# Kernel optimization log

Hardware: AMD Instinct MI355X
Metric: run time of the kernel (lower is better)

Reference implementation:

```python
import jax, jax.numpy as jnp
import numpy as np

EMBED_DIM = 2048
NUM_HEADS = 32
NUM_SEQS = 8
SEQ_LEN = 1024
TOTAL_TOKENS = NUM_SEQS * SEQ_LEN


def setup_inputs() -> dict:
    key = jax.random.key(0)
    ks = jax.random.split(key, 9)
    E = EMBED_DIM
    std = 0.02
    return {
        "hidden_states": jax.random.normal(ks[0], (TOTAL_TOKENS, E), dtype=jnp.float32),
        "Wq": jax.random.normal(ks[1], (E, E), dtype=jnp.float32) * std,
        "bq": jax.random.normal(ks[2], (E,), dtype=jnp.float32) * std,
        "Wk": jax.random.normal(ks[3], (E, E), dtype=jnp.float32) * std,
        "bk": jax.random.normal(ks[4], (E,), dtype=jnp.float32) * std,
        "Wv": jax.random.normal(ks[5], (E, E), dtype=jnp.float32) * std,
        "bv": jax.random.normal(ks[6], (E,), dtype=jnp.float32) * std,
        "Wo": jax.random.normal(ks[7], (E, E), dtype=jnp.float32) * std,
        "bo": jax.random.normal(ks[8], (E,), dtype=jnp.float32) * std,
        "seq_len": SEQ_LEN,
    }


def reference(hidden_states, Wq, bq, Wk, bk, Wv, bv, Wo, bo, seq_len):
    # OPTAttention (has_cache=False): block-diagonal causal attention over
    # packed ragged sequences; here all NUM_SEQS sequences have length seq_len,
    # so the block-diagonal mask is exactly per-sequence causal attention.
    T, E = hidden_states.shape
    H = NUM_HEADS
    D = E // H
    B = T // seq_len
    scaling = D ** -0.5

    # torch nn.Linear: y = x @ W.T + b
    q = hidden_states @ Wq.T + bq
    k = hidden_states @ Wk.T + bk
    v = hidden_states @ Wv.T + bv

    q = q.reshape(B, seq_len, H, D)
    k = k.reshape(B, seq_len, H, D)
    v = v.reshape(B, seq_len, H, D)

    # [B, H, S, S] attention scores (xformers applies scale to q@k.T)
    scores = jnp.einsum("bqhd,bkhd->bhqk", q, k) * scaling
    causal = jnp.tril(jnp.ones((seq_len, seq_len), dtype=bool))
    scores = jnp.where(causal[None, None, :, :], scores, jnp.finfo(scores.dtype).min)
    probs = jax.nn.softmax(scores, axis=-1)

    attn = jnp.einsum("bhqk,bkhd->bqhd", probs, v)  # [B, S, H, D]
    attn = attn.reshape(T, E)
    return attn @ Wo.T + bo
```

## Files before the change

### kernel.cpp

```cpp
#include <hip/hip_runtime.h>
#include <hip/hip_bf16.h>

typedef __bf16 bf16_t;
typedef __bf16 bf16x8 __attribute__((ext_vector_type(8)));
typedef __bf16 bf16x4 __attribute__((ext_vector_type(4)));
typedef float f32x4 __attribute__((ext_vector_type(4)));
typedef float f32x16 __attribute__((ext_vector_type(16)));
typedef unsigned short u16x8 __attribute__((ext_vector_type(8)));
typedef unsigned int u32x4 __attribute__((ext_vector_type(4)));

#define T_TOK 8192
#define E_DIM 2048
#define NHEAD 32
#define SEQLEN 1024
#define NSEQ 8
#define LDQ 6144

#if __has_builtin(__builtin_amdgcn_exp2f)
#define EXP2F(x) __builtin_amdgcn_exp2f(x)
#else
#define EXP2F(x) exp2f(x)
#endif

static __device__ inline unsigned cvtpk_bf16(float lo, float hi) {
    unsigned r;
    asm("v_cvt_pk_bf16_f32 %0, %1, %2" : "=v"(r) : "v"(lo), "v"(hi));
    return r;
}

static __device__ inline void plswap(unsigned &x, unsigned &y, bool lo_half) {
#if __has_builtin(__builtin_amdgcn_permlane32_swap)
    auto r = __builtin_amdgcn_permlane32_swap(x, y, false, false);
    x = r[0]; y = r[1];
#else
    unsigned xs = __shfl_xor(x, 32), ys = __shfl_xor(y, 32);
    unsigned nx = lo_half ? x : ys;
    unsigned ny = lo_half ? xs : y;
    x = nx; y = ny;
#endif
}

__global__ void cvt_all(const float* __restrict__ hid, const float* __restrict__ Wq,
                        const float* __restrict__ Wk, const float* __restrict__ Wv,
                        const float* __restrict__ Wo, bf16_t* __restrict__ hidB,
                        bf16_t* __restrict__ Wcat, bf16_t* __restrict__ WoB) {
    const int TE4 = (T_TOK * E_DIM) / 4;
    const int EE4 = (E_DIM * E_DIM) / 4;
    const float* src;
    bf16_t* dst;
    int n4, base, nb;
    const int bid = blockIdx.x;
    if (bid < 2048)      { src = hid; dst = hidB;              n4 = TE4; base = 0;    nb = 2048; }
    else if (bid < 2560) { src = Wq;  dst = Wcat;              n4 = EE4; base = 2048; nb = 512; }
    else if (bid < 3072) { src = Wk;  dst = Wcat + 4 * EE4;    n4 = EE4; base = 2560; nb = 512; }
    else if (bid < 3584) { src = Wv;  dst = Wcat + 8 * EE4;    n4 = EE4; base = 3072; nb = 512; }
    else                 { src = Wo;  dst = WoB;               n4 = EE4; base = 3584; nb = 512; }
    const int stride = nb * 256;
    for (int i = (bid - base) * 256 + threadIdx.x; i < n4; i += stride) {
        const float4 v = reinterpret_cast<const float4*>(src)[i];
        bf16x4 o;
        o[0] = (bf16_t)v.x; o[1] = (bf16_t)v.y; o[2] = (bf16_t)v.z; o[3] = (bf16_t)v.w;
        reinterpret_cast<bf16x4*>(dst)[i] = o;
    }
}

template<bool OUT_BF16>
__global__ __launch_bounds__(512, 2)
void gemm64(const bf16_t* __restrict__ A, const bf16_t* __restrict__ B,
            const float* __restrict__ b0, const float* __restrict__ b1,
            const float* __restrict__ b2, void* __restrict__ Cout,
            int M, int N, float qs, int qlim) {
    constexpr int K = 2048;
    constexpr int NK = K / 64;
    __shared__ alignas(16) unsigned char lds[131072];
    const int tid = threadIdx.x;
    const int wid = tid >> 6, l = tid & 63;
    const int cpx = gridDim.x >> 3;
    const int id = (blockIdx.x & 7) * cpx + (blockIdx.x >> 3);
    const int sb = id >> 5, si = id & 31;
    const int smw = (M >> 8) >> 3;
    const int bm = (sb % smw) * 8 + (si & 7);
    const int bn = (sb / smw) * 4 + (si >> 3);
    const int wrow = (wid >> 2) * 128, wcol = (wid & 3) * 64;
    const int lr = l & 15, lg = l >> 4;

    f32x4 acc[8][4] = {};

    const bf16_t* aBase = A + (size_t)(bm * 256) * K;
    const bf16_t* bBase = B + (size_t)(bn * 256) * K;

    const int srw = l >> 3;
    const int scb0 = (l & 7) * 16;
    auto stage = [&](int t, int buf) {
        unsigned char* base = lds + buf * 65536;
#pragma unroll
        for (int i = 0; i < 4; ++i) {
            const int chunk = wid * 4 + i;
            const int r = chunk * 8 + srw;
            const int cb = scb0 ^ ((r & 7) << 4);
            __builtin_amdgcn_global_load_lds(
                (const __attribute__((address_space(1))) void*)(aBase + (size_t)r * K + t * 64 + (cb >> 1)),
                (__attribute__((address_space(3))) void*)(base + chunk * 1024), 16, 0, 0);
        }
#pragma unroll
        for (int i = 0; i < 4; ++i) {
            const int chunk = wid * 4 + i;
            const int r = chunk * 8 + srw;
            const int cb = scb0 ^ ((r & 7) << 4);
            __builtin_amdgcn_global_load_lds(
                (const __attribute__((address_space(1))) void*)(bBase + (size_t)r * K + t * 64 + (cb >> 1)),
                (__attribute__((address_space(3))) void*)(base + 32768 + chunk * 1024), 16, 0, 0);
        }
    };

    stage(0, 0);
    asm volatile("s_waitcnt vmcnt(0)" ::: "memory");
    __builtin_amdgcn_s_barrier();

#pragma unroll 1
    for (int t = 0; t < NK; ++t) {
        if (t + 1 < NK) stage(t + 1, (t + 1) & 1);
        const unsigned char* Ab = lds + (t & 1) * 65536;
        const unsigned char* Bb = Ab + 32768;
        bf16x8 af[8][2], bfv[4][2];
#pragma unroll
        for (int n = 0; n < 4; ++n) {
            const int r = wcol + n * 16 + lr;
#pragma unroll
            for (int ks = 0; ks < 2; ++ks)
                bfv[n][ks] = *reinterpret_cast<const bf16x8*>(
                    Bb + r * 128 + (((unsigned)(ks * 64 + lg * 16)) ^ ((r & 7) << 4)));
        }
#pragma unroll
        for (int m = 0; m < 8; ++m) {
            const int r = wrow + m * 16 + lr;
#pragma unroll
            for (int ks = 0; ks < 2; ++ks)
                af[m][ks] = *reinterpret_cast<const bf16x8*>(
                    Ab + r * 128 + (((unsigned)(ks * 64 + lg * 16)) ^ ((r & 7) << 4)));
        }
        __builtin_amdgcn_s_setprio(1);
#pragma unroll
        for (int m = 0; m < 8; ++m)
#pragma unroll
            for (int n = 0; n < 4; ++n)
#pragma unroll
                for (int ks = 0; ks < 2; ++ks)
                    acc[m][n] = __builtin_amdgcn_mfma_f32_16x16x32_bf16(af[m][ks], bfv[n][ks], acc[m][n], 0, 0, 0);
        __builtin_amdgcn_s_setprio(0);
        if (t == NK - 1) break;
        asm volatile("s_waitcnt vmcnt(0)" ::: "memory");
        __builtin_amdgcn_s_barrier();
    }

    const int r0 = bm * 256 + wrow + lg * 4;
    const int c0 = bn * 256 + wcol + lr;
#pragma unroll
    for (int n = 0; n < 4; ++n) {
        const int cc = c0 + n * 16;
        const float bias = (cc < 2048) ? b0[cc] : (cc < 4096 ? b1[cc - 2048] : b2[cc - 4096]);
        const float sc2 = (cc < qlim) ? qs : 1.0f;
#pragma unroll
        for (int m = 0; m < 8; ++m)
#pragma unroll
            for (int j = 0; j < 4; ++j) {
                const int rr = r0 + m * 16 + j;
                const float v = (acc[m][n][j] + bias) * sc2;
                if (OUT_BF16) ((bf16_t*)Cout)[(size_t)rr * N + cc] = (bf16_t)v;
                else          ((float*)Cout)[(size_t)rr * N + cc] = v;
            }
    }
}

__global__ __launch_bounds__(512, 2)
void attn_fwd3(const bf16_t* __restrict__ QKV, bf16_t* __restrict__ Og) {
    const int orig = blockIdx.x;
    const int id = (orig & 7) * 64 + (orig >> 3);
    const int grp = id >> 1;
    const int pairIdx = id & 1;
    const int h = grp & 31;
    const int sq = grp >> 5;

    const int tid = threadIdx.x;
    const int w = tid >> 6;
    const int l = tid & 63;
    const int ll = l & 31;
    const int hi = l >> 5;
    const bool lo_half = (hi == 0);

    __shared__ alignas(16) unsigned char lds[65536];

    const bf16_t* Qg = QKV;
    const bf16_t* Kg = QKV + 2048;
    const bf16_t* Vg = QKV + 4096;
    const size_t kvbase = (size_t)(sq * SEQLEN) * LDQ + h * 64;

    bf16x8 vr0, vr1;
    const int vk0 = l * 2;
    const int vd0 = w * 8;

    auto stageK = [&](int kt, int buf) {
#pragma unroll
        for (int c = 0; c < 2; ++c) {
            const int o = (w * 2 + c) * 1024 + l * 16;
            const int r = o >> 7;
            const int swb = (o & 127) ^ ((r & 7) << 4);
            const bf16_t* src = Kg + kvbase + (size_t)(kt * 128 + r) * LDQ + (swb >> 1);
            __builtin_amdgcn_global_load_lds(
                (const __attribute__((address_space(1))) void*)src,
                (__attribute__((address_space(3))) void*)(lds + buf * 16384 + (w * 2 + c) * 1024),
                16, 0, 0);
        }
    };
    auto loadV = [&](int kt) {
        const bf16_t* vp = Vg + kvbase + (size_t)(kt * 128 + vk0) * LDQ + vd0;
        vr0 = *reinterpret_cast<const bf16x8*>(vp);
        vr1 = *reinterpret_cast<const bf16x8*>(vp + LDQ);
    };
    auto writeV = [&](int buf) {
        u16x8 s0 = __builtin_bit_cast(u16x8, vr0);
        u16x8 s1 = __builtin_bit_cast(u16x8, vr1);
        unsigned char* vb = lds + 32768 + buf * 16384;
#pragma unroll
        for (int e = 0; e < 8; ++e) {
            const int d = vd0 + e;
            unsigned off = (unsigned)(d * 256 + vk0 * 2);
            off ^= ((unsigned)((d ^ (d >> 4)) & 15)) << 4;
            *reinterpret_cast<unsigned*>(vb + off) = (unsigned)s0[e] | ((unsigned)s1[e] << 16);
        }
    };

    const unsigned ksw = (unsigned)((l & 7) << 4);
    const unsigned kbase = (unsigned)(ll * 128 + hi * 16);

#pragma unroll 1
    for (int seg = 0; seg < 2; ++seg) {
        const int qt = pairIdx ? (seg ? 2 : 1) : (seg ? 3 : 0);

        const int q_glob = qt * 256 + w * 32 + ll;
        const bf16_t* qp = Qg + (size_t)(sq * SEQLEN + q_glob) * LDQ + h * 64 + hi * 8;
        bf16x8 qf[4];
#pragma unroll
        for (int dc = 0; dc < 4; ++dc)
            qf[dc] = *reinterpret_cast<const bf16x8*>(qp + dc * 16);

        const int nkt = 2 * qt + 2;
        const int q_wave_max = qt * 256 + w * 32 + 31;

        f32x16 oac[2] = {};
        float mrun = -3.0e38f, lsum = 0.f;

        stageK(0, 0);
        loadV(0);
        writeV(0);
        __syncthreads();

        int cur = 0;
        for (int kt = 0; kt < nkt; ++kt) {
            const bool notlast = (kt + 1 < nkt);
            if (notlast) { stageK(kt + 1, cur ^ 1); loadV(kt + 1); }

            if (kt * 128 <= q_wave_max) {
                const unsigned char* Kcur = lds + cur * 16384;
                const unsigned char* Vcur = lds + 32768 + cur * 16384;

                f32x16 st[4];
#pragma unroll
                for (int kh = 0; kh < 4; ++kh) {
                    f32x16 acc = {};
#pragma unroll
                    for (int dc = 0; dc < 4; ++dc) {
                        const unsigned off = (kbase + (unsigned)(kh * 4096 + dc * 32)) ^ ksw;
                        const bf16x8 ka = *reinterpret_cast<const bf16x8*>(Kcur + off);
                        acc = __builtin_amdgcn_mfma_f32_32x32x16_bf16(ka, qf[dc], acc, 0, 0, 0);
                    }
                    st[kh] = acc;
                }

                if (kt >= 2 * qt) {
#pragma unroll
                    for (int kh = 0; kh < 4; ++kh)
#pragma unroll
                        for (int r = 0; r < 16; ++r) {
                            const int kg = kt * 128 + kh * 32 + (r & 3) + 8 * (r >> 2) + 4 * hi;
                            if (kg > q_glob) st[kh][r] = -3.0e38f;
                        }
                }

                float tm = -3.0e38f;
#pragma unroll
                for (int kh = 0; kh < 4; ++kh)
#pragma unroll
                    for (int r = 0; r < 16; ++r) tm = fmaxf(tm, st[kh][r]);
                tm = fmaxf(tm, __shfl_xor(tm, 32));

                if (!__all(tm <= mrun + 8.0f)) {
                    const float mnew = fmaxf(mrun, tm);
                    const float rsc = EXP2F(mrun - mnew);
                    mrun = mnew;
                    lsum *= rsc;
#pragma unroll
                    for (int dh = 0; dh < 2; ++dh)
#pragma unroll
                        for (int r = 0; r < 16; ++r) oac[dh][r] *= rsc;
                }

                float ps = 0.f;
#pragma unroll
                for (int kh = 0; kh < 4; ++kh)
#pragma unroll
                    for (int r = 0; r < 16; ++r) {
                        const float p = EXP2F(st[kh][r] - mrun);
                        st[kh][r] = p;
                        ps += p;
                    }
                ps += __shfl_xor(ps, 32);
                lsum += ps;

                bf16x8 pf[8];
#pragma unroll
                for (int kh = 0; kh < 4; ++kh)
#pragma unroll
                    for (int hc = 0; hc < 2; ++hc) {
                        const int b0i = hc * 8;
                        unsigned a  = cvtpk_bf16(st[kh][b0i + 0], st[kh][b0i + 1]);
                        unsigned b  = cvtpk_bf16(st[kh][b0i + 4], st[kh][b0i + 5]);
                        unsigned a2 = cvtpk_bf16(st[kh][b0i + 2], st[kh][b0i + 3]);
                        unsigned b2 = cvtpk_bf16(st[kh][b0i + 6], st[kh][b0i + 7]);
                        plswap(a, b, lo_half);
                        plswap(a2, b2, lo_half);
                        u32x4 words = { a, a2, b, b2 };
                        pf[kh * 2 + hc] = __builtin_bit_cast(bf16x8, words);
                    }

#pragma unroll
                for (int dh = 0; dh < 2; ++dh) {
                    const int d = dh * 32 + ll;
                    const unsigned vsw = ((unsigned)((d ^ (d >> 4)) & 15)) << 4;
                    const unsigned vbb = (unsigned)(d * 256 + hi * 16);
#pragma unroll
                    for (int kc = 0; kc < 8; ++kc) {
                        const unsigned off = (vbb + (unsigned)(kc * 32)) ^ vsw;
                        const bf16x8 vfr = *reinterpret_cast<const bf16x8*>(Vcur + off);
                        oac[dh] = __builtin_amdgcn_mfma_f32_32x32x16_bf16(vfr, pf[kc], oac[dh], 0, 0, 0);
                    }
                }
            }

            if (notlast) writeV(cur ^ 1);
            __syncthreads();
            cur ^= 1;
        }

        const float inv = 1.0f / lsum;
        bf16_t* op = Og + (size_t)(sq * SEQLEN + q_glob) * E_DIM + h * 64;
#pragma unroll
        for (int dh = 0; dh < 2; ++dh)
#pragma unroll
            for (int rq = 0; rq < 4; ++rq) {
                const int d0 = dh * 32 + 8 * rq + 4 * hi;
                bf16x4 ov;
#pragma unroll
                for (int j = 0; j < 4; ++j)
                    ov[j] = (bf16_t)(oac[dh][rq * 4 + j] * inv);
                *reinterpret_cast<bf16x4*>(op + d0) = ov;
            }
    }
}

extern "C" void kernel_launch(void* const* d_in, const int* in_sizes, int n_in,
                              void* d_out, int out_size, void* d_ws, size_t ws_size,
                              hipStream_t stream) {
    const float* hid = (const float*)d_in[0];
    const float* Wq  = (const float*)d_in[1];
    const float* bq  = (const float*)d_in[2];
    const float* Wk  = (const float*)d_in[3];
    const float* bk  = (const float*)d_in[4];
    const float* Wv  = (const float*)d_in[5];
    const float* bv  = (const float*)d_in[6];
    const float* Wo  = (const float*)d_in[7];
    const float* bo  = (const float*)d_in[8];
    float* out = (float*)d_out;

    const size_t TE = (size_t)T_TOK * E_DIM;
    const size_t EE = (size_t)E_DIM * E_DIM;

    bf16_t* ws   = (bf16_t*)d_ws;
    bf16_t* hidB = ws;
    bf16_t* qkvB = ws + TE;
    bf16_t* Wcat = qkvB + 3 * TE;
    bf16_t* WoB  = Wcat + 3 * EE;

    cvt_all<<<4096, 256, 0, stream>>>(hid, Wq, Wk, Wv, Wo, hidB, Wcat, WoB);

    const float QSCALE = 0.125f * 1.4426950408889634f;

    gemm64<true><<<dim3((T_TOK / 256) * (LDQ / 256)), 512, 0, stream>>>(
        hidB, Wcat, bq, bk, bv, qkvB, T_TOK, LDQ, QSCALE, 2048);

    attn_fwd3<<<dim3(512), 512, 0, stream>>>(qkvB, hidB);

    gemm64<false><<<dim3((T_TOK / 256) * (E_DIM / 256)), 512, 0, stream>>>(
        hidB, WoB, bo, bo, bo, out, T_TOK, E_DIM, 1.0f, 0);
}
```

Baseline: 367.0 us.

## Share K/V tiles across paired query tiles and vectorize GEMM epilogue stores

```diff
diff --git a/kernel.cpp b/kernel.cpp
--- a/kernel.cpp
+++ b/kernel.cpp
@@ -146,40 +146,51 @@
             for (int n = 0; n < 4; ++n)
 #pragma unroll
                 for (int ks = 0; ks < 2; ++ks)
-                    acc[m][n] = __builtin_amdgcn_mfma_f32_16x16x32_bf16(af[m][ks], bfv[n][ks], acc[m][n], 0, 0, 0);
+                    acc[m][n] = __builtin_amdgcn_mfma_f32_16x16x32_bf16(bfv[n][ks], af[m][ks], acc[m][n], 0, 0, 0);
         __builtin_amdgcn_s_setprio(0);
         if (t == NK - 1) break;
         asm volatile("s_waitcnt vmcnt(0)" ::: "memory");
         __builtin_amdgcn_s_barrier();
     }
 
-    const int r0 = bm * 256 + wrow + lg * 4;
-    const int c0 = bn * 256 + wcol + lr;
+    const int r0 = bm * 256 + wrow + lr;
+    const int c0 = bn * 256 + wcol + lg * 4;
 #pragma unroll
     for (int n = 0; n < 4; ++n) {
         const int cc = c0 + n * 16;
-        const float bias = (cc < 2048) ? b0[cc] : (cc < 4096 ? b1[cc - 2048] : b2[cc - 4096]);
+        const float* bp = (cc < 2048) ? (b0 + cc) : (cc < 4096 ? (b1 + cc - 2048) : (b2 + cc - 4096));
+        const float4 bb = *reinterpret_cast<const float4*>(bp);
         const float sc2 = (cc < qlim) ? qs : 1.0f;
 #pragma unroll
-        for (int m = 0; m < 8; ++m)
-#pragma unroll
-            for (int j = 0; j < 4; ++j) {
-                const int rr = r0 + m * 16 + j;
-                const float v = (acc[m][n][j] + bias) * sc2;
-                if (OUT_BF16) ((bf16_t*)Cout)[(size_t)rr * N + cc] = (bf16_t)v;
-                else          ((float*)Cout)[(size_t)rr * N + cc] = v;
-            }
+        for (int m = 0; m < 8; ++m) {
+            const int rr = r0 + m * 16;
+            const float v0 = (acc[m][n][0] + bb.x) * sc2;
+            const float v1 = (acc[m][n][1] + bb.y) * sc2;
+            const float v2 = (acc[m][n][2] + bb.z) * sc2;
+            const float v3 = (acc[m][n][3] + bb.w) * sc2;
+            if (OUT_BF16) {
+                bf16x4 ov; ov[0] = (bf16_t)v0; ov[1] = (bf16_t)v1; ov[2] = (bf16_t)v2; ov[3] = (bf16_t)v3;
+                *reinterpret_cast<bf16x4*>((bf16_t*)Cout + (size_t)rr * N + cc) = ov;
+            } else {
+                float4 ov = { v0, v1, v2, v3 };
+                *reinterpret_cast<float4*>((float*)Cout + (size_t)rr * N + cc) = ov;
+            }
+        }
     }
 }
 
 __global__ __launch_bounds__(512, 2)
-void attn_fwd3(const bf16_t* __restrict__ QKV, bf16_t* __restrict__ Og) {
+void attn_fwd5(const bf16_t* __restrict__ QKV, bf16_t* __restrict__ Og) {
     const int orig = blockIdx.x;
     const int id = (orig & 7) * 64 + (orig >> 3);
     const int grp = id >> 1;
     const int pairIdx = id & 1;
     const int h = grp & 31;
     const int sq = grp >> 5;
+    const int qtA = pairIdx ? 1 : 0;
+    const int qtB = pairIdx ? 2 : 3;
+    const int NKT = 2 * qtB + 2;
+    const int lastA = 2 * qtA + 1;
 
     const int tid = threadIdx.x;
     const int w = tid >> 6;
@@ -233,127 +244,129 @@
     const unsigned ksw = (unsigned)((l & 7) << 4);
     const unsigned kbase = (unsigned)(ll * 128 + hi * 16);
 
+    const int qgA = qtA * 256 + w * 32 + ll;
+    const int qgB = qtB * 256 + w * 32 + ll;
+    bf16x8 qfA[4], qfB[4];
+    {
+        const bf16_t* qpA = Qg + (size_t)(sq * SEQLEN + qgA) * LDQ + h * 64 + hi * 8;
+        const bf16_t* qpB = Qg + (size_t)(sq * SEQLEN + qgB) * LDQ + h * 64 + hi * 8;
+#pragma unroll
+        for (int dc = 0; dc < 4; ++dc) {
+            qfA[dc] = *reinterpret_cast<const bf16x8*>(qpA + dc * 16);
+            qfB[dc] = *reinterpret_cast<const bf16x8*>(qpB + dc * 16);
+        }
+    }
+
+    f32x16 oacA[2] = {}, oacB[2] = {};
+    float mA = -3.0e38f, lA = 0.f, mB = -3.0e38f, lB = 0.f;
+
+    auto tileCompute = [&](const bf16x8 (&qf)[4], f32x16 (&oac)[2],
+                           float &mrun, float &lsum, int q_glob, int qt, int kt,
+                           const unsigned char* Kcur, const unsigned char* Vcur) {
+        f32x16 st[4];
+#pragma unroll
+        for (int kh = 0; kh < 4; ++kh) {
+            f32x16 acc = {};
+#pragma unroll
+            for (int dc = 0; dc < 4; ++dc) {
+                const unsigned off = (kbase + (unsigned)(kh * 4096 + dc * 32)) ^ ksw;
+                const bf16x8 ka = *reinterpret_cast<const bf16x8*>(Kcur + off);
+                acc = __builtin_amdgcn_mfma_f32_32x32x16_bf16(ka, qf[dc], acc, 0, 0, 0);
+            }
+            st[kh] = acc;
+        }
+        if (kt >= 2 * qt) {
+#pragma unroll
+            for (int kh = 0; kh < 4; ++kh)
+#pragma unroll
+                for (int r = 0; r < 16; ++r) {
+                    const int kg = kt * 128 + kh * 32 + (r & 3) + 8 * (r >> 2) + 4 * hi;
+                    if (kg > q_glob) st[kh][r] = -3.0e38f;
+                }
+        }
+        float tm = -3.0e38f;
+#pragma unroll
+        for (int kh = 0; kh < 4; ++kh)
+#pragma unroll
+            for (int r = 0; r < 16; ++r) tm = fmaxf(tm, st[kh][r]);
+        tm = fmaxf(tm, __shfl_xor(tm, 32));
+        if (!__all(tm <= mrun + 8.0f)) {
+            const float mnew = fmaxf(mrun, tm);
+            const float rsc = EXP2F(mrun - mnew);
+            mrun = mnew;
+            lsum *= rsc;
+#pragma unroll
+            for (int dh = 0; dh < 2; ++dh)
+#pragma unroll
+                for (int r = 0; r < 16; ++r) oac[dh][r] *= rsc;
+        }
+        float ps = 0.f;
+#pragma unroll
+        for (int kh = 0; kh < 4; ++kh)
+#pragma unroll
+            for (int r = 0; r < 16; ++r) {
+                const float p = EXP2F(st[kh][r] - mrun);
+                st[kh][r] = p;
+                ps += p;
+            }
+        ps += __shfl_xor(ps, 32);
+        lsum += ps;
+
+        bf16x8 pf[8];
+#pragma unroll
+        for (int kh = 0; kh < 4; ++kh)
+#pragma unroll
+            for (int hc = 0; hc < 2; ++hc) {
+                const int b0i = hc * 8;
+                unsigned a  = cvtpk_bf16(st[kh][b0i + 0], st[kh][b0i + 1]);
+                unsigned b  = cvtpk_bf16(st[kh][b0i + 4], st[kh][b0i + 5]);
+                unsigned a2 = cvtpk_bf16(st[kh][b0i + 2], st[kh][b0i + 3]);
+                unsigned b2 = cvtpk_bf16(st[kh][b0i + 6], st[kh][b0i + 7]);
+                plswap(a, b, lo_half);
+                plswap(a2, b2, lo_half);
+                u32x4 words = { a, a2, b, b2 };
+                pf[kh * 2 + hc] = __builtin_bit_cast(bf16x8, words);
+            }
+#pragma unroll
+        for (int dh = 0; dh < 2; ++dh) {
+            const int d = dh * 32 + ll;
+            const unsigned vsw = ((unsigned)((d ^ (d >> 4)) & 15)) << 4;
+            const unsigned vbb = (unsigned)(d * 256 + hi * 16);
+#pragma unroll
+            for (int kc = 0; kc < 8; ++kc) {
+                const unsigned off = (vbb + (unsigned)(kc * 32)) ^ vsw;
+                const bf16x8 vfr = *reinterpret_cast<const bf16x8*>(Vcur + off);
+                oac[dh] = __builtin_amdgcn_mfma_f32_32x32x16_bf16(vfr, pf[kc], oac[dh], 0, 0, 0);
+            }
+        }
+    };
+
+    stageK(0, 0);
+    loadV(0);
+    writeV(0);
+    __syncthreads();
+
+    int cur = 0;
 #pragma unroll 1
-    for (int seg = 0; seg < 2; ++seg) {
-        const int qt = pairIdx ? (seg ? 2 : 1) : (seg ? 3 : 0);
-
-        const int q_glob = qt * 256 + w * 32 + ll;
-        const bf16_t* qp = Qg + (size_t)(sq * SEQLEN + q_glob) * LDQ + h * 64 + hi * 8;
-        bf16x8 qf[4];
-#pragma unroll
-        for (int dc = 0; dc < 4; ++dc)
-            qf[dc] = *reinterpret_cast<const bf16x8*>(qp + dc * 16);
-
-        const int nkt = 2 * qt + 2;
-        const int q_wave_max = qt * 256 + w * 32 + 31;
-
-        f32x16 oac[2] = {};
-        float mrun = -3.0e38f, lsum = 0.f;
-
-        stageK(0, 0);
-        loadV(0);
-        writeV(0);
+    for (int kt = 0; kt < NKT; ++kt) {
+        const bool notlast = (kt + 1 < NKT);
+        if (notlast) { stageK(kt + 1, cur ^ 1); loadV(kt + 1); }
+        const unsigned char* Kcur = lds + cur * 16384;
+        const unsigned char* Vcur = lds + 32768 + cur * 16384;
+
+        if (kt * 128 <= qtB * 256 + w * 32 + 31)
+            tileCompute(qfB, oacB, mB, lB, qgB, qtB, kt, Kcur, Vcur);
+        if (kt <= lastA && kt * 128 <= qtA * 256 + w * 32 + 31)
+            tileCompute(qfA, oacA, mA, lA, qgA, qtA, kt, Kcur, Vcur);
+
+        if (notlast) writeV(cur ^ 1);
         __syncthreads();
-
-        int cur = 0;
-        for (int kt = 0; kt < nkt; ++kt) {
-            const bool notlast = (kt + 1 < nkt);
-            if (notlast) { stageK(kt + 1, cur ^ 1); loadV(kt + 1); }
-
-            if (kt * 128 <= q_wave_max) {
-                const unsigned char* Kcur = lds + cur * 16384;
-                const unsigned char* Vcur = lds + 32768 + cur * 16384;
-
-                f32x16 st[4];
-#pragma unroll
-                for (int kh = 0; kh < 4; ++kh) {
-                    f32x16 acc = {};
-#pragma unroll
-                    for (int dc = 0; dc < 4; ++dc) {
-                        const unsigned off = (kbase + (unsigned)(kh * 4096 + dc * 32)) ^ ksw;
-                        const bf16x8 ka = *reinterpret_cast<const bf16x8*>(Kcur + off);
-                        acc = __builtin_amdgcn_mfma_f32_32x32x16_bf16(ka, qf[dc], acc, 0, 0, 0);
-                    }
-                    st[kh] = acc;
-                }
-
-                if (kt >= 2 * qt) {
-#pragma unroll
-                    for (int kh = 0; kh < 4; ++kh)
-#pragma unroll
-                        for (int r = 0; r < 16; ++r) {
-                            const int kg = kt * 128 + kh * 32 + (r & 3) + 8 * (r >> 2) + 4 * hi;
-                            if (kg > q_glob) st[kh][r] = -3.0e38f;
-                        }
-                }
-
-                float tm = -3.0e38f;
-#pragma unroll
-                for (int kh = 0; kh < 4; ++kh)
-#pragma unroll
-                    for (int r = 0; r < 16; ++r) tm = fmaxf(tm, st[kh][r]);
-                tm = fmaxf(tm, __shfl_xor(tm, 32));
-
-                if (!__all(tm <= mrun + 8.0f)) {
-                    const float mnew = fmaxf(mrun, tm);
-                    const float rsc = EXP2F(mrun - mnew);
-                    mrun = mnew;
-                    lsum *= rsc;
-#pragma unroll
-                    for (int dh = 0; dh < 2; ++dh)
-#pragma unroll
-                        for (int r = 0; r < 16; ++r) oac[dh][r] *= rsc;
-                }
-
-                float ps = 0.f;
-#pragma unroll
-                for (int kh = 0; kh < 4; ++kh)
-#pragma unroll
-                    for (int r = 0; r < 16; ++r) {
-                        const float p = EXP2F(st[kh][r] - mrun);
-                        st[kh][r] = p;
-                        ps += p;
-                    }
-                ps += __shfl_xor(ps, 32);
-                lsum += ps;
-
-                bf16x8 pf[8];
-#pragma unroll
-                for (int kh = 0; kh < 4; ++kh)
-#pragma unroll
-                    for (int hc = 0; hc < 2; ++hc) {
-                        const int b0i = hc * 8;
-                        unsigned a  = cvtpk_bf16(st[kh][b0i + 0], st[kh][b0i + 1]);
-                        unsigned b  = cvtpk_bf16(st[kh][b0i + 4], st[kh][b0i + 5]);
-                        unsigned a2 = cvtpk_bf16(st[kh][b0i + 2], st[kh][b0i + 3]);
-                        unsigned b2 = cvtpk_bf16(st[kh][b0i + 6], st[kh][b0i + 7]);
-                        plswap(a, b, lo_half);
-                        plswap(a2, b2, lo_half);
-                        u32x4 words = { a, a2, b, b2 };
-                        pf[kh * 2 + hc] = __builtin_bit_cast(bf16x8, words);
-                    }
-
-#pragma unroll
-                for (int dh = 0; dh < 2; ++dh) {
-                    const int d = dh * 32 + ll;
-                    const unsigned vsw = ((unsigned)((d ^ (d >> 4)) & 15)) << 4;
-                    const unsigned vbb = (unsigned)(d * 256 + hi * 16);
-#pragma unroll
-                    for (int kc = 0; kc < 8; ++kc) {
-                        const unsigned off = (vbb + (unsigned)(kc * 32)) ^ vsw;
-                        const bf16x8 vfr = *reinterpret_cast<const bf16x8*>(Vcur + off);
-                        oac[dh] = __builtin_amdgcn_mfma_f32_32x32x16_bf16(vfr, pf[kc], oac[dh], 0, 0, 0);
-                    }
-                }
-            }
-
-            if (notlast) writeV(cur ^ 1);
-            __syncthreads();
-            cur ^= 1;
-        }
-
-        const float inv = 1.0f / lsum;
-        bf16_t* op = Og + (size_t)(sq * SEQLEN + q_glob) * E_DIM + h * 64;
+        cur ^= 1;
+    }
+
+    {
+        const float inv = 1.0f / lA;
+        bf16_t* op = Og + (size_t)(sq * SEQLEN + qgA) * E_DIM + h * 64;
 #pragma unroll
         for (int dh = 0; dh < 2; ++dh)
 #pragma unroll
@@ -362,7 +375,22 @@
                 bf16x4 ov;
 #pragma unroll
                 for (int j = 0; j < 4; ++j)
-                    ov[j] = (bf16_t)(oac[dh][rq * 4 + j] * inv);
+                    ov[j] = (bf16_t)(oacA[dh][rq * 4 + j] * inv);
+                *reinterpret_cast<bf16x4*>(op + d0) = ov;
+            }
+    }
+    {
+        const float inv = 1.0f / lB;
+        bf16_t* op = Og + (size_t)(sq * SEQLEN + qgB) * E_DIM + h * 64;
+#pragma unroll
+        for (int dh = 0; dh < 2; ++dh)
+#pragma unroll
+            for (int rq = 0; rq < 4; ++rq) {
+                const int d0 = dh * 32 + 8 * rq + 4 * hi;
+                bf16x4 ov;
+#pragma unroll
+                for (int j = 0; j < 4; ++j)
+                    ov[j] = (bf16_t)(oacB[dh][rq * 4 + j] * inv);
                 *reinterpret_cast<bf16x4*>(op + d0) = ov;
             }
     }
@@ -398,7 +426,7 @@
     gemm64<true><<<dim3((T_TOK / 256) * (LDQ / 256)), 512, 0, stream>>>(
         hidB, Wcat, bq, bk, bv, qkvB, T_TOK, LDQ, QSCALE, 2048);
 
-    attn_fwd3<<<dim3(512), 512, 0, stream>>>(qkvB, hidB);
+    attn_fwd5<<<dim3(512), 512, 0, stream>>>(qkvB, hidB);
 
     gemm64<false><<<dim3((T_TOK / 256) * (E_DIM / 256)), 512, 0, stream>>>(
         hidB, WoB, bo, bo, bo, out, T_TOK, E_DIM, 1.0f, 0);
```

Result: slower. 389.9 us (+6.2%).
